# Optimization experiments

Hardware: AMD Instinct MI355X
Metric: run time of the kernel (lower is better)

Reference implementation:

```python
import jax, jax.numpy as jnp
import numpy as np

N = 100000   # num_nodes
E = 1600000  # num_edges
DIN = 128
H1 = 256
H2 = 128
SLOPE = 0.01  # torch leaky_relu default negative slope


def _gcn_conv(h, W, b, src, dst):
    # GCNConv: add self-loops, symmetric deg^-1/2 normalization, linear transform, scatter-add, bias
    hw = h @ W  # [N, out]
    loops = jnp.arange(N)
    s = jnp.concatenate([src, loops])
    d = jnp.concatenate([dst, loops])
    deg = jax.ops.segment_sum(jnp.ones(s.shape[0], dtype=hw.dtype), d, num_segments=N)
    dis = jnp.where(deg > 0, jax.lax.rsqrt(deg), 0.0)
    msg = hw[s] * (dis[s] * dis[d])[:, None]
    return jax.ops.segment_sum(msg, d, num_segments=N) + b


def _gru_cell(x, h, Wih, Whh, bih, bhh):
    # torch.nn.GRUCell semantics; weight layout [3H, in], gate order r, z, n
    gi = x @ Wih.T + bih
    gh = h @ Whh.T + bhh
    ir, iz, inn = jnp.split(gi, 3, axis=-1)
    hr, hz, hn = jnp.split(gh, 3, axis=-1)
    r = jax.nn.sigmoid(ir + hr)
    z = jax.nn.sigmoid(iz + hz)
    n = jnp.tanh(inn + r * hn)
    return (1.0 - z) * n + z * h


def setup_inputs() -> dict:
    key = jax.random.key(0)
    ks = jax.random.split(key, 24)
    rn = lambda k, shape, s=0.05: (jax.random.normal(k, shape) * s).astype(jnp.float32)
    return {
        "x": rn(ks[0], (N, DIN), 1.0),
        "edge_index": jax.random.randint(ks[1], (2, E), 0, N, dtype=jnp.int32),
        "prev0": rn(ks[2], (N, H1), 1.0),
        "prev1": rn(ks[3], (N, H2), 1.0),
        "Wp1": rn(ks[4], (DIN, 256)), "bp1": jnp.zeros((256,), jnp.float32),
        "Wp2": rn(ks[5], (256, 128)), "bp2": jnp.zeros((128,), jnp.float32),
        "Wc1": rn(ks[6], (128, H1)), "bc1": jnp.zeros((H1,), jnp.float32),
        "Wc2": rn(ks[7], (H1, H2)), "bc2": jnp.zeros((H2,), jnp.float32),
        "Wih1": rn(ks[8], (3 * H1, H1)), "Whh1": rn(ks[9], (3 * H1, H1)),
        "bih1": jnp.zeros((3 * H1,), jnp.float32), "bhh1": jnp.zeros((3 * H1,), jnp.float32),
        "Wih2": rn(ks[10], (3 * H2, H2)), "Whh2": rn(ks[11], (3 * H2, H2)),
        "bih2": jnp.zeros((3 * H2,), jnp.float32), "bhh2": jnp.zeros((3 * H2,), jnp.float32),
        "Wpost": rn(ks[12], (H2, 2)), "bpost": jnp.zeros((2,), jnp.float32),
    }


def reference(x, edge_index, prev0, prev1, Wp1, bp1, Wp2, bp2, Wc1, bc1, Wc2, bc2,
              Wih1, Whh1, bih1, bhh1, Wih2, Whh2, bih2, bhh2, Wpost, bpost):
    src, dst = edge_index[0], edge_index[1]
    # preprocess MLP (dropout p=0 => identity)
    h = jax.nn.leaky_relu(x @ Wp1 + bp1, SLOPE)
    h = jax.nn.leaky_relu(h @ Wp2 + bp2, SLOPE)
    # GCN layer 1 + GRU temporal update
    h = jax.nn.leaky_relu(_gcn_conv(h, Wc1, bc1, src, dst), SLOPE)
    h = _gru_cell(h, prev0, Wih1, Whh1, bih1, bhh1)
    emb0 = h
    # GCN layer 2 + GRU temporal update
    h = jax.nn.leaky_relu(_gcn_conv(h, Wc2, bc2, src, dst), SLOPE)
    h = _gru_cell(h, prev1, Wih2, Whh2, bih2, bhh2)
    emb1 = h
    # postprocess and reduce
    out = jnp.sum(h @ Wpost + bpost, axis=-1)  # [N]
    return out, emb0, emb1
```

## Files before the change

kernel.cpp:

```cpp
#include <hip/hip_runtime.h>
#include <cstdint>
#include <cstddef>

typedef __bf16 bf16x8 __attribute__((ext_vector_type(8)));
typedef float f32x4 __attribute__((ext_vector_type(4)));
typedef unsigned short us16;

__device__ __forceinline__ float lrelu(float v) { return v >= 0.0f ? v : 0.01f * v; }
__device__ __forceinline__ float fsigmoid(float x) {
  x = fminf(fmaxf(x, -30.0f), 30.0f);
  return 1.0f / (1.0f + __expf(-x));
}
__device__ __forceinline__ float ftanh(float x) {
  x = fminf(fmaxf(x, -15.0f), 15.0f);
  float e = __expf(2.0f * x);
  return (e - 1.0f) / (e + 1.0f);
}
__device__ __forceinline__ us16 f2b(float f) {
  unsigned int u = __builtin_bit_cast(unsigned int, f);
  u = (u + 0x7fffu + ((u >> 16) & 1u)) >> 16;
  return (us16)u;
}
__device__ __forceinline__ float b2f(us16 h) {
  unsigned int u = ((unsigned int)h) << 16;
  return __builtin_bit_cast(float, u);
}
__device__ __forceinline__ void unp8(int4 v, float* t) {
  unsigned a = (unsigned)v.x, b = (unsigned)v.y, c = (unsigned)v.z, d = (unsigned)v.w;
  t[0] = b2f((us16)(a & 0xffff)); t[1] = b2f((us16)(a >> 16));
  t[2] = b2f((us16)(b & 0xffff)); t[3] = b2f((us16)(b >> 16));
  t[4] = b2f((us16)(c & 0xffff)); t[5] = b2f((us16)(c >> 16));
  t[6] = b2f((us16)(d & 0xffff)); t[7] = b2f((us16)(d >> 16));
}

__global__ void k_deg(const int* __restrict__ dst, int* __restrict__ indeg, int E) {
  int e = blockIdx.x * 256 + threadIdx.x;
  if (e < E) atomicAdd(&indeg[dst[e]], 1);
}

__global__ void k_dis(const int* __restrict__ indeg, float* __restrict__ dis, int n) {
  int i = blockIdx.x * 256 + threadIdx.x;
  if (i < n) dis[i] = rsqrtf((float)(indeg[i] + 1));
}

__global__ __launch_bounds__(1024) void k_scan1(const int* __restrict__ v, int* __restrict__ rp,
                                                int* __restrict__ part, int n) {
  __shared__ int wsum[16];
  int base = blockIdx.x << 10;
  int t = threadIdx.x, lane = t & 63, wv = t >> 6;
  int val = (base + t < n) ? v[base + t] : 0;
  int s = val;
  #pragma unroll
  for (int off = 1; off < 64; off <<= 1) {
    int u = __shfl_up(s, off);
    if (lane >= off) s += u;
  }
  if (lane == 63) wsum[wv] = s;
  __syncthreads();
  int wadd = 0;
  #pragma unroll
  for (int w = 0; w < 16; ++w) wadd += (w < wv) ? wsum[w] : 0;
  if (base + t < n) rp[base + t] = wadd + s - val;
  if (t == 0) {
    int tot = 0;
    #pragma unroll
    for (int w = 0; w < 16; ++w) tot += wsum[w];
    part[blockIdx.x] = tot;
  }
}

__global__ __launch_bounds__(1024) void k_scan2(int* __restrict__ p, int nc) {
  __shared__ int wsum[16];
  int t = threadIdx.x, lane = t & 63, wv = t >> 6;
  int val = (t < nc) ? p[t] : 0;
  int s = val;
  #pragma unroll
  for (int off = 1; off < 64; off <<= 1) {
    int u = __shfl_up(s, off);
    if (lane >= off) s += u;
  }
  if (lane == 63) wsum[wv] = s;
  __syncthreads();
  int wadd = 0;
  #pragma unroll
  for (int w = 0; w < 16; ++w) wadd += (w < wv) ? wsum[w] : 0;
  if (t < nc) p[t] = wadd + s - val;
}

__global__ void k_scan3(int* __restrict__ rp, const int* __restrict__ part, int n, int total) {
  int i = blockIdx.x * 256 + threadIdx.x;
  if (i < n) rp[i] += part[i >> 10];
  else if (i == n) rp[n] = total;
}

__global__ void k_fill(const int* __restrict__ src, const int* __restrict__ dst,
                       const float* __restrict__ dis, int* __restrict__ cursor,
                       int* __restrict__ csrc, float* __restrict__ cw, int E) {
  int e = blockIdx.x * 256 + threadIdx.x;
  if (e >= E) return;
  int s = src[e], d = dst[e];
  int pos = atomicAdd(&cursor[d], 1);
  csrc[pos] = s;
  cw[pos] = dis[s] * dis[d];
}

__global__ void k_cast(const float* __restrict__ in, us16* __restrict__ out, int n) {
  int i = (blockIdx.x * 256 + threadIdx.x) * 4;
  if (i >= n) return;
  float4 v = *(const float4*)(in + i);
  *(ushort4*)(out + i) = make_ushort4(f2b(v.x), f2b(v.y), f2b(v.z), f2b(v.w));
}

__global__ void k_tpose(const float* __restrict__ in, us16* __restrict__ out, int R, int C) {
  int t = blockIdx.x * 256 + threadIdx.x;
  if (t >= R * C) return;
  int r = t % R, c = t / R;
  out[(size_t)c * R + r] = f2b(in[(size_t)r * C + c]);
}

template<int ACT, int BIAS>
__global__ __launch_bounds__(256) void k_mm(const us16* __restrict__ A,
                                            const us16* __restrict__ Bt,
                                            const float* __restrict__ bias,
                                            us16* __restrict__ Cb,
                                            int M, int K, int Nc, int ny) {
  __shared__ __align__(16) us16 As[128 * 72];
  __shared__ __align__(16) us16 Bs[128 * 72];
  const int bm = (blockIdx.x / ny) * 128;
  const int bn = (blockIdx.x % ny) * 128;
  const int tid = threadIdx.x;
  const int lane = tid & 63;
  const int wave = tid >> 6;
  const int wm = (wave >> 1) * 64;
  const int wn = (wave & 1) * 64;
  const int lr = lane & 15;
  const int lk = lane >> 4;
  const int sr = tid >> 3;
  const int sc = (tid & 7) * 8;
  f32x4 acc[4][4] = {};
  for (int k0 = 0; k0 < K; k0 += 64) {
    #pragma unroll
    for (int it = 0; it < 4; ++it) {
      int r = sr + it * 32;
      int gr = bm + r;
      int4 va = make_int4(0, 0, 0, 0);
      if (gr < M) va = *(const int4*)(A + (size_t)gr * K + k0 + sc);
      *(int4*)(&As[r * 72 + sc]) = va;
      int4 vb = *(const int4*)(Bt + (size_t)(bn + r) * K + k0 + sc);
      *(int4*)(&Bs[r * 72 + sc]) = vb;
    }
    __syncthreads();
    #pragma unroll
    for (int kk = 0; kk < 2; ++kk) {
      bf16x8 af[4], bq[4];
      #pragma unroll
      for (int i = 0; i < 4; ++i)
        af[i] = *(const bf16x8*)(&As[(wm + i * 16 + lr) * 72 + kk * 32 + lk * 8]);
      #pragma unroll
      for (int j = 0; j < 4; ++j)
        bq[j] = *(const bf16x8*)(&Bs[(wn + j * 16 + lr) * 72 + kk * 32 + lk * 8]);
      #pragma unroll
      for (int i = 0; i < 4; ++i)
        #pragma unroll
        for (int j = 0; j < 4; ++j)
          acc[i][j] = __builtin_amdgcn_mfma_f32_16x16x32_bf16(af[i], bq[j], acc[i][j], 0, 0, 0);
    }
    __syncthreads();
  }
  float bb[4];
  #pragma unroll
  for (int j = 0; j < 4; ++j) bb[j] = BIAS ? bias[bn + wn + j * 16 + lr] : 0.0f;
  #pragma unroll
  for (int i = 0; i < 4; ++i) {
    #pragma unroll
    for (int q = 0; q < 4; ++q) {
      int row = bm + wm + i * 16 + lk * 4 + q;
      if (row < M) {
        #pragma unroll
        for (int j = 0; j < 4; ++j) {
          int col = bn + wn + j * 16 + lr;
          float v = acc[i][j][q] + bb[j];
          if (ACT) v = lrelu(v);
          Cb[(size_t)row * Nc + col] = f2b(v);
        }
      }
    }
  }
}

template<int ACT>
__global__ __launch_bounds__(256) void k_agg128(const us16* __restrict__ hw, const int* __restrict__ rp,
                                                const int* __restrict__ csrc, const float* __restrict__ cw,
                                                const float* __restrict__ dis, const float* __restrict__ bias,
                                                us16* __restrict__ outp, int M) {
  int node = blockIdx.x * 16 + (threadIdx.x >> 4);
  int l = threadIdx.x & 15;
  if (node >= M) return;
  const us16* base = hw + l * 8;
  float acc[8], t0[8], t1[8];
  float dn = dis[node];
  float sw = dn * dn;
  {
    int4 v = *(const int4*)(base + (size_t)node * 128);
    unp8(v, t0);
    #pragma unroll
    for (int j = 0; j < 8; ++j) acc[j] = t0[j] * sw;
  }
  int e = rp[node], e1 = rp[node + 1];
  for (; e + 2 <= e1; e += 2) {
    int s0 = csrc[e], s1 = csrc[e + 1];
    float w0 = cw[e], w1 = cw[e + 1];
    int4 v0 = *(const int4*)(base + (size_t)s0 * 128);
    int4 v1 = *(const int4*)(base + (size_t)s1 * 128);
    unp8(v0, t0);
    unp8(v1, t1);
    #pragma unroll
    for (int j = 0; j < 8; ++j) acc[j] = fmaf(w0, t0[j], acc[j]);
    #pragma unroll
    for (int j = 0; j < 8; ++j) acc[j] = fmaf(w1, t1[j], acc[j]);
  }
  if (e < e1) {
    int s0 = csrc[e];
    float w0 = cw[e];
    int4 v0 = *(const int4*)(base + (size_t)s0 * 128);
    unp8(v0, t0);
    #pragma unroll
    for (int j = 0; j < 8; ++j) acc[j] = fmaf(w0, t0[j], acc[j]);
  }
  if (ACT) {
    float4 b0 = *(const float4*)(bias + l * 8);
    float4 b1 = *(const float4*)(bias + l * 8 + 4);
    float bb[8] = {b0.x, b0.y, b0.z, b0.w, b1.x, b1.y, b1.z, b1.w};
    #pragma unroll
    for (int j = 0; j < 8; ++j) acc[j] = lrelu(acc[j] + bb[j]);
  }
  int4 o;
  o.x = (int)((unsigned)f2b(acc[0]) | ((unsigned)f2b(acc[1]) << 16));
  o.y = (int)((unsigned)f2b(acc[2]) | ((unsigned)f2b(acc[3]) << 16));
  o.z = (int)((unsigned)f2b(acc[4]) | ((unsigned)f2b(acc[5]) << 16));
  o.w = (int)((unsigned)f2b(acc[6]) | ((unsigned)f2b(acc[7]) << 16));
  *(int4*)(outp + (size_t)node * 128 + l * 8) = o;
}

template<int H, int WB, int NY>
__global__ __launch_bounds__(256) void k_fgru(const us16* __restrict__ xb, const us16* __restrict__ hb,
                                              const us16* __restrict__ Wih, const us16* __restrict__ Whh,
                                              const float* __restrict__ bih, const float* __restrict__ bhh,
                                              float* __restrict__ emb, us16* __restrict__ embb, int M) {
  constexpr int LDW = 40;
  __shared__ __align__(16) us16 xs[64 * LDW];
  __shared__ __align__(16) us16 hs[64 * LDW];
  __shared__ __align__(16) us16 ws[6][64 * LDW];
  const int bn = (blockIdx.x % NY) * 64;
  const int bm = (blockIdx.x / NY) * 64;
  const int tid = threadIdx.x;
  const int lane = tid & 63, wave = tid >> 6;
  const int wm = (wave >> 1) * 32, wn = (wave & 1) * 32;
  const int lr = lane & 15, lk = lane >> 4;
  const int srow = tid >> 2;
  const int scol = (tid & 3) * 8;
  f32x4 acc[6][2][2] = {};
  const bool rv = (bm + srow) < M;
  const us16* xrp = xb + (size_t)(bm + srow) * H;
  const us16* hrp = hb + (size_t)(bm + srow) * H;

  for (int k0 = 0; k0 < H; k0 += 32) {
    int4 vx = rv ? *(const int4*)(xrp + k0 + scol) : make_int4(0, 0, 0, 0);
    int4 vh = rv ? *(const int4*)(hrp + k0 + scol) : make_int4(0, 0, 0, 0);
    *(int4*)(xs + srow * LDW + scol) = vx;
    *(int4*)(hs + srow * LDW + scol) = vh;
    #pragma unroll
    for (int g = 0; g < 3; ++g) {
      int4 wi = *(const int4*)(Wih + (size_t)(g * H + bn + srow) * H + k0 + scol);
      *(int4*)(ws[g] + srow * LDW + scol) = wi;
      int4 wh = *(const int4*)(Whh + (size_t)(g * H + bn + srow) * H + k0 + scol);
      *(int4*)(ws[3 + g] + srow * LDW + scol) = wh;
    }
    __syncthreads();
    bf16x8 ax[2], ah[2];
    #pragma unroll
    for (int i = 0; i < 2; ++i) {
      ax[i] = *(const bf16x8*)(xs + (wm + i * 16 + lr) * LDW + lk * 8);
      ah[i] = *(const bf16x8*)(hs + (wm + i * 16 + lr) * LDW + lk * 8);
    }
    #pragma unroll
    for (int g = 0; g < 6; ++g) {
      bf16x8 bq[2];
      #pragma unroll
      for (int j = 0; j < 2; ++j)
        bq[j] = *(const bf16x8*)(ws[g] + (wn + j * 16 + lr) * LDW + lk * 8);
      #pragma unroll
      for (int i = 0; i < 2; ++i)
        #pragma unroll
        for (int j = 0; j < 2; ++j)
          acc[g][i][j] = __builtin_amdgcn_mfma_f32_16x16x32_bf16(
              (g < 3 ? ax[i] : ah[i]), bq[j], acc[g][i][j], 0, 0, 0);
    }
    __syncthreads();
  }
  #pragma unroll
  for (int j = 0; j < 2; ++j) {
    int col = bn + wn + j * 16 + lr;
    float bir = bih[col], biz = bih[H + col], bin = bih[2 * H + col];
    float bhr = bhh[col], bhz = bhh[H + col], bhn = bhh[2 * H + col];
    #pragma unroll
    for (int i = 0; i < 2; ++i) {
      #pragma unroll
      for (int q = 0; q < 4; ++q) {
        int row = bm + wm + i * 16 + lk * 4 + q;
        if (row >= M) continue;
        float r = fsigmoid(acc[0][i][j][q] + bir + acc[3][i][j][q] + bhr);
        float z = fsigmoid(acc[1][i][j][q] + biz + acc[4][i][j][q] + bhz);
        float n = ftanh(acc[2][i][j][q] + bin + r * (acc[5][i][j][q] + bhn));
        float hv = b2f(hb[(size_t)row * H + col]);
        float o = (1.0f - z) * n + z * hv;
        emb[(size_t)row * H + col] = o;
        if (WB) embb[(size_t)row * H + col] = f2b(o);
      }
    }
  }
}

__global__ __launch_bounds__(256) void k_post(const float* __restrict__ emb, const float* __restrict__ Wpost,
                                              const float* __restrict__ bpost, float* __restrict__ outv, int M) {
  int gw = (int)((blockIdx.x * 256 + threadIdx.x) >> 6);
  int lane = threadIdx.x & 63;
  if (gw >= M) return;
  float2 ev = *(const float2*)(emb + (size_t)gw * 128 + lane * 2);
  float4 wv = *(const float4*)(Wpost + lane * 4);
  float p = ev.x * (wv.x + wv.y) + ev.y * (wv.z + wv.w);
  #pragma unroll
  for (int o = 32; o > 0; o >>= 1) p += __shfl_xor(p, o);
  if (lane == 0) outv[gw] = p + bpost[0] + bpost[1];
}

extern "C" void kernel_launch(void* const* d_in, const int* in_sizes, int n_in,
                              void* d_out, int out_size, void* d_ws, size_t ws_size,
                              hipStream_t stream) {
  const float* x     = (const float*)d_in[0];
  const int*   ei    = (const int*)d_in[1];
  const float* prev0 = (const float*)d_in[2];
  const float* prev1 = (const float*)d_in[3];
  const float* Wp1   = (const float*)d_in[4];
  const float* bp1   = (const float*)d_in[5];
  const float* Wp2   = (const float*)d_in[6];
  const float* bp2   = (const float*)d_in[7];
  const float* Wc1   = (const float*)d_in[8];
  const float* bc1   = (const float*)d_in[9];
  const float* Wc2   = (const float*)d_in[10];
  const float* bc2   = (const float*)d_in[11];
  const float* Wih1  = (const float*)d_in[12];
  const float* Whh1  = (const float*)d_in[13];
  const float* bih1  = (const float*)d_in[14];
  const float* bhh1  = (const float*)d_in[15];
  const float* Wih2  = (const float*)d_in[16];
  const float* Whh2  = (const float*)d_in[17];
  const float* bih2  = (const float*)d_in[18];
  const float* bhh2  = (const float*)d_in[19];
  const float* Wpost = (const float*)d_in[20];
  const float* bpost = (const float*)d_in[21];

  const int N = in_sizes[0] / 128;
  const int E = in_sizes[1] / 2;
  const int* srcp = ei;
  const int* dstp = ei + E;

  char* wsb = (char*)d_ws;
  size_t off = 0;
  auto alloc = [&](size_t bytes) -> void* {
    void* p = wsb + off;
    off = (off + bytes + 255) & ~(size_t)255;
    return p;
  };
  float* dis    = (float*)alloc((size_t)N * 4);
  int*   indeg  = (int*)alloc((size_t)N * 4);
  int*   rp     = (int*)alloc((size_t)(N + 1) * 4);
  int*   part   = (int*)alloc((size_t)1024 * 4);
  int*   cursor = (int*)alloc((size_t)N * 4);
  int*   csrc   = (int*)alloc((size_t)E * 4);
  float* cw     = (float*)alloc((size_t)E * 4);
  us16* xb    = (us16*)alloc((size_t)N * 128 * 2);
  us16* p0b   = (us16*)alloc((size_t)N * 256 * 2);
  us16* p1b   = (us16*)alloc((size_t)N * 128 * 2);
  us16* WtP1  = (us16*)alloc((size_t)256 * 128 * 2);
  us16* WtP2  = (us16*)alloc((size_t)128 * 256 * 2);
  us16* WtC1  = (us16*)alloc((size_t)256 * 128 * 2);
  us16* WtC2  = (us16*)alloc((size_t)128 * 256 * 2);
  us16* Wih1b = (us16*)alloc((size_t)768 * 256 * 2);
  us16* Whh1b = (us16*)alloc((size_t)768 * 256 * 2);
  us16* Wih2b = (us16*)alloc((size_t)384 * 128 * 2);
  us16* Whh2b = (us16*)alloc((size_t)384 * 128 * 2);
  us16* bufA  = (us16*)alloc((size_t)N * 256 * 2);
  us16* bufB  = (us16*)alloc((size_t)N * 128 * 2);
  us16* bufD  = (us16*)alloc((size_t)N * 128 * 2);
  us16* emb0b = (us16*)alloc((size_t)N * 256 * 2);
  (void)ws_size; (void)n_in; (void)out_size;

  float* outv = (float*)d_out;
  float* emb0 = outv + N;
  float* emb1 = emb0 + (size_t)N * 256;

  auto cg = [](long n) { return (unsigned)((n / 4 + 255) / 256); };

  k_cast<<<cg((long)N * 128), 256, 0, stream>>>(x, xb, N * 128);
  k_cast<<<cg((long)N * 256), 256, 0, stream>>>(prev0, p0b, N * 256);
  k_cast<<<cg((long)N * 128), 256, 0, stream>>>(prev1, p1b, N * 128);
  k_cast<<<cg(768 * 256), 256, 0, stream>>>(Wih1, Wih1b, 768 * 256);
  k_cast<<<cg(768 * 256), 256, 0, stream>>>(Whh1, Whh1b, 768 * 256);
  k_cast<<<cg(384 * 128), 256, 0, stream>>>(Wih2, Wih2b, 384 * 128);
  k_cast<<<cg(384 * 128), 256, 0, stream>>>(Whh2, Whh2b, 384 * 128);
  k_tpose<<<(128 * 256 + 255) / 256, 256, 0, stream>>>(Wp1, WtP1, 128, 256);
  k_tpose<<<(256 * 128 + 255) / 256, 256, 0, stream>>>(Wp2, WtP2, 256, 128);
  k_tpose<<<(128 * 256 + 255) / 256, 256, 0, stream>>>(Wc1, WtC1, 128, 256);
  k_tpose<<<(256 * 128 + 255) / 256, 256, 0, stream>>>(Wc2, WtC2, 256, 128);

  hipMemsetAsync(indeg, 0, (size_t)N * 4, stream);
  k_deg<<<(E + 255) / 256, 256, 0, stream>>>(dstp, indeg, E);
  k_dis<<<(N + 255) / 256, 256, 0, stream>>>(indeg, dis, N);
  const int NC = (N + 1023) / 1024;
  k_scan1<<<NC, 1024, 0, stream>>>(indeg, rp, part, N);
  k_scan2<<<1, 1024, 0, stream>>>(part, NC);
  k_scan3<<<(N + 256) / 256, 256, 0, stream>>>(rp, part, N, E);
  hipMemcpyAsync(cursor, rp, (size_t)N * 4, hipMemcpyDeviceToDevice, stream);
  k_fill<<<(E + 255) / 256, 256, 0, stream>>>(srcp, dstp, dis, cursor, csrc, cw, E);

  const int MB = (N + 127) / 128;
  const int FB = (N + 63) / 64;
  const int AB = (N + 15) / 16;

  k_mm<1, 1><<<MB * 2, 256, 0, stream>>>(xb, WtP1, bp1, bufA, N, 128, 256, 2);
  k_mm<1, 1><<<MB, 256, 0, stream>>>(bufA, WtP2, bp2, bufB, N, 256, 128, 1);
  k_agg128<0><<<AB, 256, 0, stream>>>(bufB, rp, csrc, cw, dis, nullptr, bufD, N);
  k_mm<1, 1><<<MB * 2, 256, 0, stream>>>(bufD, WtC1, bc1, bufA, N, 128, 256, 2);
  k_fgru<256, 1, 4><<<FB * 4, 256, 0, stream>>>(bufA, p0b, Wih1b, Whh1b, bih1, bhh1,
                                                emb0, emb0b, N);
  k_mm<0, 0><<<MB, 256, 0, stream>>>(emb0b, WtC2, nullptr, bufB, N, 256, 128, 1);
  k_agg128<1><<<AB, 256, 0, stream>>>(bufB, rp, csrc, cw, dis, bc2, bufD, N);
  k_fgru<128, 0, 2><<<FB * 2, 256, 0, stream>>>(bufD, p1b, Wih2b, Whh2b, bih2, bhh2,
                                                emb1, nullptr, N);
  k_post<<<(N + 3) / 4, 256, 0, stream>>>(emb1, Wpost, bpost, outv, N);
}
```

Before: 818.6 us.

## Use direct global-to-LDS loads with XOR swizzle; restructure fused GRU into two passes

The GEMM and fused GRU kernels now stage tiles through global_load_lds with an XOR-swizzled 64-wide LDS layout in place of padded register round-trips. The GRU kernel moves to 128-row tiles and runs the input-gate and hidden-gate products as two sequential K loops. It keeps the input-gate results packed as bf16 in registers, which cuts LDS footprint and doubles rows per block. The aggregation loop is unrolled to four edges to put more gathers in flight. The trade-offs are extra bf16 rounding of the gate pre-activations and higher register pressure.

Measured after the change: 896.7 us. 9.6% more time.

```diff
diff --git a/kernel.cpp b/kernel.cpp
--- a/kernel.cpp
+++ b/kernel.cpp
@@ -24,6 +24,9 @@
 __device__ __forceinline__ float b2f(us16 h) {
   unsigned int u = ((unsigned int)h) << 16;
   return __builtin_bit_cast(float, u);
+}
+__device__ __forceinline__ unsigned pk2(float a, float b) {
+  return (unsigned)f2b(a) | ((unsigned)f2b(b) << 16);
 }
 __device__ __forceinline__ void unp8(int4 v, float* t) {
   unsigned a = (unsigned)v.x, b = (unsigned)v.y, c = (unsigned)v.z, d = (unsigned)v.w;
@@ -31,6 +34,16 @@
   t[2] = b2f((us16)(b & 0xffff)); t[3] = b2f((us16)(b >> 16));
   t[4] = b2f((us16)(c & 0xffff)); t[5] = b2f((us16)(c >> 16));
   t[6] = b2f((us16)(d & 0xffff)); t[7] = b2f((us16)(d >> 16));
+}
+
+__device__ __forceinline__ void stage16(const us16* gsrc, us16* ldst) {
+  __builtin_amdgcn_global_load_lds(
+      (const __attribute__((address_space(1))) unsigned int*)(const void*)gsrc,
+      (__attribute__((address_space(3))) unsigned int*)(void*)ldst, 16, 0, 0);
+}
+__device__ __forceinline__ bf16x8 frag_rd(const us16* base, int row, int byte_in_row) {
+  int byte = row * 128 + (byte_in_row ^ ((row & 7) << 4));
+  return *(const bf16x8*)((const char*)base + byte);
 }
 
 __global__ void k_deg(const int* __restrict__ dst, int* __restrict__ indeg, int E) {
@@ -124,8 +137,8 @@
                                             const float* __restrict__ bias,
                                             us16* __restrict__ Cb,
                                             int M, int K, int Nc, int ny) {
-  __shared__ __align__(16) us16 As[128 * 72];
-  __shared__ __align__(16) us16 Bs[128 * 72];
+  __shared__ __align__(16) us16 As[128 * 64];
+  __shared__ __align__(16) us16 Bs[128 * 64];
   const int bm = (blockIdx.x / ny) * 128;
   const int bn = (blockIdx.x % ny) * 128;
   const int tid = threadIdx.x;
@@ -135,30 +148,25 @@
   const int wn = (wave & 1) * 64;
   const int lr = lane & 15;
   const int lk = lane >> 4;
-  const int sr = tid >> 3;
-  const int sc = (tid & 7) * 8;
+  const int srow = lane >> 3;
+  const int schk = (lane & 7) ^ srow;
   f32x4 acc[4][4] = {};
   for (int k0 = 0; k0 < K; k0 += 64) {
     #pragma unroll
     for (int it = 0; it < 4; ++it) {
-      int r = sr + it * 32;
-      int gr = bm + r;
-      int4 va = make_int4(0, 0, 0, 0);
-      if (gr < M) va = *(const int4*)(A + (size_t)gr * K + k0 + sc);
-      *(int4*)(&As[r * 72 + sc]) = va;
-      int4 vb = *(const int4*)(Bt + (size_t)(bn + r) * K + k0 + sc);
-      *(int4*)(&Bs[r * 72 + sc]) = vb;
+      int r8 = (wave * 4 + it) * 8;
+      int ar = bm + r8 + srow; if (ar >= M) ar = M - 1;
+      stage16(A + (size_t)ar * K + k0 + schk * 8, As + r8 * 64);
+      stage16(Bt + (size_t)(bn + r8 + srow) * K + k0 + schk * 8, Bs + r8 * 64);
     }
     __syncthreads();
     #pragma unroll
     for (int kk = 0; kk < 2; ++kk) {
       bf16x8 af[4], bq[4];
       #pragma unroll
-      for (int i = 0; i < 4; ++i)
-        af[i] = *(const bf16x8*)(&As[(wm + i * 16 + lr) * 72 + kk * 32 + lk * 8]);
-      #pragma unroll
-      for (int j = 0; j < 4; ++j)
-        bq[j] = *(const bf16x8*)(&Bs[(wn + j * 16 + lr) * 72 + kk * 32 + lk * 8]);
+      for (int i = 0; i < 4; ++i) af[i] = frag_rd(As, wm + i * 16 + lr, kk * 64 + lk * 16);
+      #pragma unroll
+      for (int j = 0; j < 4; ++j) bq[j] = frag_rd(Bs, wn + j * 16 + lr, kk * 64 + lk * 16);
       #pragma unroll
       for (int i = 0; i < 4; ++i)
         #pragma unroll
@@ -197,7 +205,7 @@
   int l = threadIdx.x & 15;
   if (node >= M) return;
   const us16* base = hw + l * 8;
-  float acc[8], t0[8], t1[8];
+  float acc[8], t0[8], t1[8], t2[8], t3[8];
   float dn = dis[node];
   float sw = dn * dn;
   {
@@ -207,19 +215,24 @@
     for (int j = 0; j < 8; ++j) acc[j] = t0[j] * sw;
   }
   int e = rp[node], e1 = rp[node + 1];
-  for (; e + 2 <= e1; e += 2) {
-    int s0 = csrc[e], s1 = csrc[e + 1];
-    float w0 = cw[e], w1 = cw[e + 1];
+  for (; e + 4 <= e1; e += 4) {
+    int s0 = csrc[e], s1 = csrc[e + 1], s2 = csrc[e + 2], s3 = csrc[e + 3];
+    float w0 = cw[e], w1 = cw[e + 1], w2 = cw[e + 2], w3 = cw[e + 3];
     int4 v0 = *(const int4*)(base + (size_t)s0 * 128);
     int4 v1 = *(const int4*)(base + (size_t)s1 * 128);
-    unp8(v0, t0);
-    unp8(v1, t1);
+    int4 v2 = *(const int4*)(base + (size_t)s2 * 128);
+    int4 v3 = *(const int4*)(base + (size_t)s3 * 128);
+    unp8(v0, t0); unp8(v1, t1); unp8(v2, t2); unp8(v3, t3);
     #pragma unroll
     for (int j = 0; j < 8; ++j) acc[j] = fmaf(w0, t0[j], acc[j]);
     #pragma unroll
     for (int j = 0; j < 8; ++j) acc[j] = fmaf(w1, t1[j], acc[j]);
-  }
-  if (e < e1) {
+    #pragma unroll
+    for (int j = 0; j < 8; ++j) acc[j] = fmaf(w2, t2[j], acc[j]);
+    #pragma unroll
+    for (int j = 0; j < 8; ++j) acc[j] = fmaf(w3, t3[j], acc[j]);
+  }
+  for (; e < e1; ++e) {
     int s0 = csrc[e];
     float w0 = cw[e];
     int4 v0 = *(const int4*)(base + (size_t)s0 * 128);
@@ -235,83 +248,142 @@
     for (int j = 0; j < 8; ++j) acc[j] = lrelu(acc[j] + bb[j]);
   }
   int4 o;
-  o.x = (int)((unsigned)f2b(acc[0]) | ((unsigned)f2b(acc[1]) << 16));
-  o.y = (int)((unsigned)f2b(acc[2]) | ((unsigned)f2b(acc[3]) << 16));
-  o.z = (int)((unsigned)f2b(acc[4]) | ((unsigned)f2b(acc[5]) << 16));
-  o.w = (int)((unsigned)f2b(acc[6]) | ((unsigned)f2b(acc[7]) << 16));
+  o.x = (int)pk2(acc[0], acc[1]);
+  o.y = (int)pk2(acc[2], acc[3]);
+  o.z = (int)pk2(acc[4], acc[5]);
+  o.w = (int)pk2(acc[6], acc[7]);
   *(int4*)(outp + (size_t)node * 128 + l * 8) = o;
 }
 
-template<int H, int WB, int NY>
+template<int H, int WB>
 __global__ __launch_bounds__(256) void k_fgru(const us16* __restrict__ xb, const us16* __restrict__ hb,
                                               const us16* __restrict__ Wih, const us16* __restrict__ Whh,
                                               const float* __restrict__ bih, const float* __restrict__ bhh,
-                                              float* __restrict__ emb, us16* __restrict__ embb, int M) {
-  constexpr int LDW = 40;
-  __shared__ __align__(16) us16 xs[64 * LDW];
-  __shared__ __align__(16) us16 hs[64 * LDW];
-  __shared__ __align__(16) us16 ws[6][64 * LDW];
-  const int bn = (blockIdx.x % NY) * 64;
-  const int bm = (blockIdx.x / NY) * 64;
+                                              float* __restrict__ emb, us16* __restrict__ embb,
+                                              int M, int ny) {
+  __shared__ __align__(16) us16 as_[128 * 64];
+  __shared__ __align__(16) us16 ws[3 * 64 * 64];
+  const int bn = (blockIdx.x % ny) * 64;
+  const int bm = (blockIdx.x / ny) * 128;
   const int tid = threadIdx.x;
   const int lane = tid & 63, wave = tid >> 6;
-  const int wm = (wave >> 1) * 32, wn = (wave & 1) * 32;
+  const int wm = (wave >> 1) * 64, wn = (wave & 1) * 32;
   const int lr = lane & 15, lk = lane >> 4;
-  const int srow = tid >> 2;
-  const int scol = (tid & 3) * 8;
-  f32x4 acc[6][2][2] = {};
-  const bool rv = (bm + srow) < M;
-  const us16* xrp = xb + (size_t)(bm + srow) * H;
-  const us16* hrp = hb + (size_t)(bm + srow) * H;
-
-  for (int k0 = 0; k0 < H; k0 += 32) {
-    int4 vx = rv ? *(const int4*)(xrp + k0 + scol) : make_int4(0, 0, 0, 0);
-    int4 vh = rv ? *(const int4*)(hrp + k0 + scol) : make_int4(0, 0, 0, 0);
-    *(int4*)(xs + srow * LDW + scol) = vx;
-    *(int4*)(hs + srow * LDW + scol) = vh;
-    #pragma unroll
-    for (int g = 0; g < 3; ++g) {
-      int4 wi = *(const int4*)(Wih + (size_t)(g * H + bn + srow) * H + k0 + scol);
-      *(int4*)(ws[g] + srow * LDW + scol) = wi;
-      int4 wh = *(const int4*)(Whh + (size_t)(g * H + bn + srow) * H + k0 + scol);
-      *(int4*)(ws[3 + g] + srow * LDW + scol) = wh;
+  const int srow = lane >> 3;
+  const int schk = (lane & 7) ^ srow;
+
+  f32x4 acc[3][4][2];
+  #pragma unroll
+  for (int g = 0; g < 3; ++g)
+    #pragma unroll
+    for (int i = 0; i < 4; ++i)
+      #pragma unroll
+      for (int j = 0; j < 2; ++j) acc[g][i][j] = {0.f, 0.f, 0.f, 0.f};
+
+  for (int k0 = 0; k0 < H; k0 += 64) {
+    #pragma unroll
+    for (int it = 0; it < 4; ++it) {
+      int r8 = (wave * 4 + it) * 8;
+      int ar = bm + r8 + srow; if (ar >= M) ar = M - 1;
+      stage16(xb + (size_t)ar * H + k0 + schk * 8, as_ + r8 * 64);
+    }
+    #pragma unroll
+    for (int it = 0; it < 6; ++it) {
+      int idx = wave * 6 + it;
+      int g = idx >> 3, rr = (idx & 7) * 8;
+      stage16(Wih + (size_t)(g * H + bn + rr + srow) * H + k0 + schk * 8,
+              ws + g * 64 * 64 + rr * 64);
     }
     __syncthreads();
-    bf16x8 ax[2], ah[2];
-    #pragma unroll
-    for (int i = 0; i < 2; ++i) {
-      ax[i] = *(const bf16x8*)(xs + (wm + i * 16 + lr) * LDW + lk * 8);
-      ah[i] = *(const bf16x8*)(hs + (wm + i * 16 + lr) * LDW + lk * 8);
-    }
-    #pragma unroll
-    for (int g = 0; g < 6; ++g) {
-      bf16x8 bq[2];
-      #pragma unroll
-      for (int j = 0; j < 2; ++j)
-        bq[j] = *(const bf16x8*)(ws[g] + (wn + j * 16 + lr) * LDW + lk * 8);
-      #pragma unroll
-      for (int i = 0; i < 2; ++i)
+    #pragma unroll
+    for (int kk = 0; kk < 2; ++kk) {
+      bf16x8 a[4], bq[3][2];
+      #pragma unroll
+      for (int i = 0; i < 4; ++i) a[i] = frag_rd(as_, wm + i * 16 + lr, kk * 64 + lk * 16);
+      #pragma unroll
+      for (int g = 0; g < 3; ++g)
         #pragma unroll
         for (int j = 0; j < 2; ++j)
-          acc[g][i][j] = __builtin_amdgcn_mfma_f32_16x16x32_bf16(
-              (g < 3 ? ax[i] : ah[i]), bq[j], acc[g][i][j], 0, 0, 0);
+          bq[g][j] = frag_rd(ws + g * 64 * 64, wn + j * 16 + lr, kk * 64 + lk * 16);
+      #pragma unroll
+      for (int g = 0; g < 3; ++g)
+        #pragma unroll
+        for (int i = 0; i < 4; ++i)
+          #pragma unroll
+          for (int j = 0; j < 2; ++j)
+            acc[g][i][j] = __builtin_amdgcn_mfma_f32_16x16x32_bf16(a[i], bq[g][j], acc[g][i][j], 0, 0, 0);
+    }
+    __syncthreads();
+  }
+  uint2 pgi[3][4][2];
+  #pragma unroll
+  for (int g = 0; g < 3; ++g)
+    #pragma unroll
+    for (int i = 0; i < 4; ++i)
+      #pragma unroll
+      for (int j = 0; j < 2; ++j) {
+        pgi[g][i][j].x = pk2(acc[g][i][j][0], acc[g][i][j][1]);
+        pgi[g][i][j].y = pk2(acc[g][i][j][2], acc[g][i][j][3]);
+        acc[g][i][j] = {0.f, 0.f, 0.f, 0.f};
+      }
+  for (int k0 = 0; k0 < H; k0 += 64) {
+    #pragma unroll
+    for (int it = 0; it < 4; ++it) {
+      int r8 = (wave * 4 + it) * 8;
+      int ar = bm + r8 + srow; if (ar >= M) ar = M - 1;
+      stage16(hb + (size_t)ar * H + k0 + schk * 8, as_ + r8 * 64);
+    }
+    #pragma unroll
+    for (int it = 0; it < 6; ++it) {
+      int idx = wave * 6 + it;
+      int g = idx >> 3, rr = (idx & 7) * 8;
+      stage16(Whh + (size_t)(g * H + bn + rr + srow) * H + k0 + schk * 8,
+              ws + g * 64 * 64 + rr * 64);
+    }
+    __syncthreads();
+    #pragma unroll
+    for (int kk = 0; kk < 2; ++kk) {
+      bf16x8 a[4], bq[3][2];
+      #pragma unroll
+      for (int i = 0; i < 4; ++i) a[i] = frag_rd(as_, wm + i * 16 + lr, kk * 64 + lk * 16);
+      #pragma unroll
+      for (int g = 0; g < 3; ++g)
+        #pragma unroll
+        for (int j = 0; j < 2; ++j)
+          bq[g][j] = frag_rd(ws + g * 64 * 64, wn + j * 16 + lr, kk * 64 + lk * 16);
+      #pragma unroll
+      for (int g = 0; g < 3; ++g)
+        #pragma unroll
+        for (int i = 0; i < 4; ++i)
+          #pragma unroll
+          for (int j = 0; j < 2; ++j)
+            acc[g][i][j] = __builtin_amdgcn_mfma_f32_16x16x32_bf16(a[i], bq[g][j], acc[g][i][j], 0, 0, 0);
     }
     __syncthreads();
   }
   #pragma unroll
   for (int j = 0; j < 2; ++j) {
     int col = bn + wn + j * 16 + lr;
-    float bir = bih[col], biz = bih[H + col], bin = bih[2 * H + col];
-    float bhr = bhh[col], bhz = bhh[H + col], bhn = bhh[2 * H + col];
-    #pragma unroll
-    for (int i = 0; i < 2; ++i) {
+    float sr = bih[col] + bhh[col];
+    float sz = bih[H + col] + bhh[H + col];
+    float bni = bih[2 * H + col];
+    float bnh = bhh[2 * H + col];
+    #pragma unroll
+    for (int i = 0; i < 4; ++i) {
       #pragma unroll
       for (int q = 0; q < 4; ++q) {
         int row = bm + wm + i * 16 + lk * 4 + q;
         if (row >= M) continue;
-        float r = fsigmoid(acc[0][i][j][q] + bir + acc[3][i][j][q] + bhr);
-        float z = fsigmoid(acc[1][i][j][q] + biz + acc[4][i][j][q] + bhz);
-        float n = ftanh(acc[2][i][j][q] + bin + r * (acc[5][i][j][q] + bhn));
+        unsigned w0 = (q & 2) ? pgi[0][i][j].y : pgi[0][i][j].x;
+        unsigned w1 = (q & 2) ? pgi[1][i][j].y : pgi[1][i][j].x;
+        unsigned w2 = (q & 2) ? pgi[2][i][j].y : pgi[2][i][j].x;
+        int sh = (q & 1) * 16;
+        float gir = b2f((us16)(w0 >> sh));
+        float giz = b2f((us16)(w1 >> sh));
+        float gin = b2f((us16)(w2 >> sh));
+        float r = fsigmoid(gir + acc[0][i][j][q] + sr);
+        float z = fsigmoid(giz + acc[1][i][j][q] + sz);
+        float n = ftanh(gin + bni + r * (acc[2][i][j][q] + bnh));
         float hv = b2f(hb[(size_t)row * H + col]);
         float o = (1.0f - z) * n + z * hv;
         emb[(size_t)row * H + col] = o;
@@ -425,18 +497,17 @@
   k_fill<<<(E + 255) / 256, 256, 0, stream>>>(srcp, dstp, dis, cursor, csrc, cw, E);
 
   const int MB = (N + 127) / 128;
-  const int FB = (N + 63) / 64;
   const int AB = (N + 15) / 16;
 
   k_mm<1, 1><<<MB * 2, 256, 0, stream>>>(xb, WtP1, bp1, bufA, N, 128, 256, 2);
   k_mm<1, 1><<<MB, 256, 0, stream>>>(bufA, WtP2, bp2, bufB, N, 256, 128, 1);
   k_agg128<0><<<AB, 256, 0, stream>>>(bufB, rp, csrc, cw, dis, nullptr, bufD, N);
   k_mm<1, 1><<<MB * 2, 256, 0, stream>>>(bufD, WtC1, bc1, bufA, N, 128, 256, 2);
-  k_fgru<256, 1, 4><<<FB * 4, 256, 0, stream>>>(bufA, p0b, Wih1b, Whh1b, bih1, bhh1,
-                                                emb0, emb0b, N);
+  k_fgru<256, 1><<<MB * 4, 256, 0, stream>>>(bufA, p0b, Wih1b, Whh1b, bih1, bhh1,
+                                             emb0, emb0b, N, 4);
   k_mm<0, 0><<<MB, 256, 0, stream>>>(emb0b, WtC2, nullptr, bufB, N, 256, 128, 1);
   k_agg128<1><<<AB, 256, 0, stream>>>(bufB, rp, csrc, cw, dis, bc2, bufD, N);
-  k_fgru<128, 0, 2><<<FB * 2, 256, 0, stream>>>(bufD, p1b, Wih2b, Whh2b, bih2, bhh2,
-                                                emb1, nullptr, N);
+  k_fgru<128, 0><<<MB * 2, 256, 0, stream>>>(bufD, p1b, Wih2b, Whh2b, bih2, bhh2,
+                                             emb1, nullptr, N, 2);
   k_post<<<(N + 3) / 4, 256, 0, stream>>>(emb1, Wpost, bpost, outv, N);
 }
```
